# Kernel optimization log

Measured on AMD Instinct MI355X. Metric: run time of the kernel, lower is better.

Reference implementation:

```python
import jax, jax.numpy as jnp
import numpy as np

HIDDEN = 64

def gcn_conv(x, W, b, src, dst, num_nodes):
    # GCNConv: out = D^{-1/2} (A + I) D^{-1/2} (x @ W) + b
    h = x @ W                                            # [N, F_out]
    ones = jnp.ones(src.shape[0], dtype=x.dtype)
    deg = jax.ops.segment_sum(ones, dst, num_segments=num_nodes) + 1.0  # +1 for self-loop
    dinv = jax.lax.rsqrt(deg)                             # deg^{-1/2}, deg >= 1 so safe
    norm = dinv[src] * dinv[dst]                          # [E]
    msgs = h[src] * norm[:, None]                         # [E, F_out]
    agg = jax.ops.segment_sum(msgs, dst, num_segments=num_nodes)
    # self-loop contribution: norm for (i,i) edge = dinv[i]^2
    out = agg + h * (dinv * dinv)[:, None] + b
    return out


def setup_inputs() -> dict:
    key = jax.random.key(0)
    k1, k2, k3, k4, k5 = jax.random.split(key, 5)
    N, F_in, F_out, E = 50000, 256, 128, 1600000
    x = jax.random.normal(k1, (N, F_in), dtype=jnp.float32)
    edge_index = jax.random.randint(k2, (2, E), 0, N, dtype=jnp.int64)
    W1 = jax.random.normal(k3, (F_in, HIDDEN), dtype=jnp.float32) * (1.0 / np.sqrt(F_in))
    b1 = jnp.zeros((HIDDEN,), dtype=jnp.float32)
    W2 = jax.random.normal(k4, (HIDDEN, F_out), dtype=jnp.float32) * (1.0 / np.sqrt(HIDDEN))
    b2 = jnp.zeros((F_out,), dtype=jnp.float32)
    return {"x": x, "edge_index": edge_index, "W1": W1, "b1": b1, "W2": W2, "b2": b2}


def reference(x, edge_index, W1, b1, W2, b2):
    num_nodes = x.shape[0]
    src, dst = edge_index[0], edge_index[1]
    h = gcn_conv(x, W1, b1, src, dst, num_nodes)
    h = jax.nn.relu(h)
    # dropout is identity in eval mode (training=False)
    out = gcn_conv(h, W2, b2, src, dst, num_nodes)
    return out
```

## Files before the change

kernel.cpp:

```cpp
#include <hip/hip_runtime.h>

#define FI 256
#define FH 64
#define FO 128
#define ASORT_CHUNK 2048

__device__ __forceinline__ ushort f2bf(float x) {
    unsigned b = __float_as_uint(x);
    b += 0x7fffu + ((b >> 16) & 1u);
    return (ushort)(b >> 16);
}
__device__ __forceinline__ float bf2f(ushort u) {
    return __uint_as_float(((unsigned)u) << 16);
}


__global__ void zero_i32(int* __restrict__ p, int n) {
    int i = blockIdx.x * 256 + threadIdx.x;
    if (i < n) p[i] = 0;
}

__global__ void deg_cnt_kernel(const int* __restrict__ dst, int* __restrict__ cnt, int E) {
    int base = blockIdx.x * 1024 + threadIdx.x;
    #pragma unroll
    for (int q = 0; q < 4; ++q) {
        int e = base + q * 256;
        if (e < E) atomicAdd(&cnt[dst[e]], 1);
    }
}

__global__ void dinv_kernel(const int* __restrict__ cnt, float* __restrict__ dinv, int N) {
    int i = blockIdx.x * 256 + threadIdx.x;
    if (i < N) dinv[i] = rsqrtf((float)cnt[i] + 1.0f);
}


__global__ __launch_bounds__(256) void hist_part_kernel(const int* __restrict__ dst,
                                                        int* __restrict__ bucket_cnt, int E) {
    __shared__ int lcnt[256];
    int t = threadIdx.x;
    int base = blockIdx.x * ASORT_CHUNK;
    lcnt[t] = 0;
    __syncthreads();
    #pragma unroll
    for (int j = 0; j < 8; ++j) {
        int e = base + j * 256 + t;
        if (e < E) atomicAdd(&lcnt[((unsigned)dst[e]) >> 8], 1);
    }
    __syncthreads();
    int v = lcnt[t];
    if (v > 0) atomicAdd(&bucket_cnt[t], v);
}

__global__ __launch_bounds__(256) void bucket_scan_kernel(const int* __restrict__ bucket_cnt,
                                                          int* __restrict__ bucket_base,
                                                          int* __restrict__ bucket_pos, int E) {
    __shared__ int sc[256];
    int t = threadIdx.x;
    int sum = bucket_cnt[t];
    sc[t] = sum;
    __syncthreads();
    for (int off = 1; off < 256; off <<= 1) {
        int u = (t >= off) ? sc[t - off] : 0;
        __syncthreads();
        sc[t] += u;
        __syncthreads();
    }
    int excl = sc[t] - sum;
    bucket_base[t] = excl;
    bucket_pos[t]  = excl;
    if (t == 255) bucket_base[256] = sc[255];
}

__global__ __launch_bounds__(256) void binA_kernel(const int* __restrict__ src,
                                                   const int* __restrict__ dst,
                                                   int* __restrict__ bucket_pos,
                                                   unsigned* __restrict__ binned, int E) {
    __shared__ int lcnt[256];
    __shared__ int lbase[256];
    __shared__ int gbase[256];
    __shared__ int sc[256];
    __shared__ unsigned sorted[ASORT_CHUNK];
    int t = threadIdx.x;
    int base = blockIdx.x * ASORT_CHUNK;
    lcnt[t] = 0;
    __syncthreads();
    unsigned pk[8];
    short bb[8];
    short mi[8];
    #pragma unroll
    for (int j = 0; j < 8; ++j) {
        int e = base + j * 256 + t;
        if (e < E) {
            unsigned s = (unsigned)src[e];
            unsigned d = (unsigned)dst[e];
            pk[j] = s | (d << 16);
            int b = (int)(d >> 8);
            bb[j] = (short)b;
            mi[j] = (short)atomicAdd(&lcnt[b], 1);
        } else {
            bb[j] = -1;
        }
    }
    __syncthreads();
    int v = lcnt[t];
    sc[t] = v;
    __syncthreads();
    #pragma unroll
    for (int off = 1; off < 256; off <<= 1) {
        int u = (t >= off) ? sc[t - off] : 0;
        __syncthreads();
        sc[t] += u;
        __syncthreads();
    }
    lbase[t] = sc[t] - v;
    if (v > 0) gbase[t] = atomicAdd(&bucket_pos[t], v);
    __syncthreads();
    #pragma unroll
    for (int j = 0; j < 8; ++j)
        if (bb[j] >= 0) sorted[lbase[(int)bb[j]] + (int)mi[j]] = pk[j];
    int tot = sc[255];
    __syncthreads();
    for (int i = t; i < tot; i += 256) {
        unsigned vv = sorted[i];
        int b = (int)(vv >> 24);
        binned[gbase[b] + (i - lbase[b])] = vv;
    }
}

__global__ __launch_bounds__(256) void binB_kernel(const int* __restrict__ bucket_base,
                                                   const unsigned* __restrict__ binned,
                                                   int* __restrict__ rec4,
                                                   int* __restrict__ row_start,
                                                   int* __restrict__ cnt,
                                                   float* __restrict__ dinv, int N) {
    __shared__ int lcnt[256];
    __shared__ int sc[256];
    __shared__ int lstart[256];
    __shared__ int loff[256];
    int t = threadIdx.x;
    int d0 = blockIdx.x << 8;
    int start = bucket_base[blockIdx.x];
    int end   = bucket_base[blockIdx.x + 1];
    lcnt[t] = 0;
    __syncthreads();
    for (int i = start + t; i < end; i += 256)
        atomicAdd(&lcnt[(binned[i] >> 16) & 0xffu], 1);
    __syncthreads();
    int v = lcnt[t];
    sc[t] = v;
    __syncthreads();
    for (int off = 1; off < 256; off <<= 1) {
        int u = (t >= off) ? sc[t - off] : 0;
        __syncthreads();
        sc[t] += u;
        __syncthreads();
    }
    int st = start + sc[t] - v;
    lstart[t] = st;
    loff[t] = 0;
    if (d0 + t < N) {
        row_start[d0 + t] = st;
        cnt[d0 + t] = v;
        dinv[d0 + t] = rsqrtf((float)v + 1.0f);
    }
    __syncthreads();
    int i = start + t;
    for (; i + 768 < end; i += 1024) {
        unsigned v0 = binned[i];
        unsigned v1 = binned[i + 256];
        unsigned v2 = binned[i + 512];
        unsigned v3 = binned[i + 768];
        int dA = (int)((v0 >> 16) & 0xffu); int kA = atomicAdd(&loff[dA], 1);
        rec4[lstart[dA] + kA] = (int)(v0 & 0xffffu);
        int dB = (int)((v1 >> 16) & 0xffu); int kB = atomicAdd(&loff[dB], 1);
        rec4[lstart[dB] + kB] = (int)(v1 & 0xffffu);
        int dC = (int)((v2 >> 16) & 0xffu); int kC = atomicAdd(&loff[dC], 1);
        rec4[lstart[dC] + kC] = (int)(v2 & 0xffffu);
        int dD = (int)((v3 >> 16) & 0xffu); int kD = atomicAdd(&loff[dD], 1);
        rec4[lstart[dD] + kD] = (int)(v3 & 0xffffu);
    }
    for (; i < end; i += 256) {
        unsigned v4 = binned[i];
        int d = (int)((v4 >> 16) & 0xffu);
        int k = atomicAdd(&loff[d], 1);
        rec4[lstart[d] + k] = (int)(v4 & 0xffffu);
    }
}


#define ACC8(hv, wt)                                                   \
    acc[0] = fmaf(__uint_as_float((hv).x << 16),         wt, acc[0]);  \
    acc[1] = fmaf(__uint_as_float((hv).x & 0xffff0000u), wt, acc[1]);  \
    acc[2] = fmaf(__uint_as_float((hv).y << 16),         wt, acc[2]);  \
    acc[3] = fmaf(__uint_as_float((hv).y & 0xffff0000u), wt, acc[3]);  \
    acc[4] = fmaf(__uint_as_float((hv).z << 16),         wt, acc[4]);  \
    acc[5] = fmaf(__uint_as_float((hv).z & 0xffff0000u), wt, acc[5]);  \
    acc[6] = fmaf(__uint_as_float((hv).w << 16),         wt, acc[6]);  \
    acc[7] = fmaf(__uint_as_float((hv).w & 0xffff0000u), wt, acc[7]);

#define GATHER_CHUNK(OFFS)                                                     \
    for (int c0 = 0; c0 < n; c0 += 64) {                                       \
        int idx_l = c0 + L;                                                    \
        int sreg = node;                                                       \
        float wreg = 0.f;                                                      \
        if (idx_l < n) {                                                       \
            sreg = rec4[beg + idx_l];                                          \
            wreg = dinv[sreg] * dvd;                                           \
        }                                                                      \
        int m = n - c0; if (m > 64) m = 64;                                    \
        int umax = (m + 7) >> 3;                                               \
        uint4 hv[8];                                                           \
        _Pragma("unroll")                                                      \
        for (int u = 0; u < 8; ++u) {                                          \
            if (u < umax) {                                                    \
                int sidx = __shfl(sreg, u * 8 + g, 64);                        \
                hv[u] = *(const uint4*)(hb + (size_t)sidx * 256 + (OFFS) + q * 8); \
            }                                                                  \
        }                                                                      \
        _Pragma("unroll")                                                      \
        for (int u = 0; u < 8; ++u) {                                          \
            if (u < umax) {                                                    \
                float wt = __shfl(wreg, u * 8 + g, 64);                        \
                ACC8(hv[u], wt)                                                \
            }                                                                  \
        }                                                                      \
    }

__global__ void gather_relu_kernel(const int* __restrict__ rec4, const int* __restrict__ row_start,
                                   const int* __restrict__ cnt, const float* __restrict__ dinv,
                                   const float* __restrict__ b1, float* __restrict__ out, int N) {
    int node = blockIdx.x * 4 + (threadIdx.x >> 6);
    if (node >= N) return;
    int L = threadIdx.x & 63;
    int g = L >> 3;
    int q = L & 7;
    const ushort* hb = (const ushort*)out;
    int beg = row_start[node];
    int n   = cnt[node];
    float dvd = dinv[node];
    float acc[8] = {0.f, 0.f, 0.f, 0.f, 0.f, 0.f, 0.f, 0.f};
    GATHER_CHUNK(128)
    #pragma unroll
    for (int off = 8; off < 64; off <<= 1)
        #pragma unroll
        for (int j = 0; j < 8; ++j)
            acc[j] += __shfl_xor(acc[j], off, 64);
    if (L < 8) {
        float dv2 = dvd * dvd;
        uint4 ho = *(const uint4*)(hb + (size_t)node * 256 + 128 + q * 8);
        float4 bl = *(const float4*)&b1[q * 8];
        float4 bh = *(const float4*)&b1[q * 8 + 4];
        float r0 = fmaxf(acc[0] + dv2 * __uint_as_float(ho.x << 16)         + bl.x, 0.f);
        float r1 = fmaxf(acc[1] + dv2 * __uint_as_float(ho.x & 0xffff0000u) + bl.y, 0.f);
        float r2 = fmaxf(acc[2] + dv2 * __uint_as_float(ho.y << 16)         + bl.z, 0.f);
        float r3 = fmaxf(acc[3] + dv2 * __uint_as_float(ho.y & 0xffff0000u) + bl.w, 0.f);
        float r4 = fmaxf(acc[4] + dv2 * __uint_as_float(ho.z << 16)         + bh.x, 0.f);
        float r5 = fmaxf(acc[5] + dv2 * __uint_as_float(ho.z & 0xffff0000u) + bh.y, 0.f);
        float r6 = fmaxf(acc[6] + dv2 * __uint_as_float(ho.w << 16)         + bh.z, 0.f);
        float r7 = fmaxf(acc[7] + dv2 * __uint_as_float(ho.w & 0xffff0000u) + bh.w, 0.f);
        uint4 st;
        st.x = (unsigned)f2bf(r0) | ((unsigned)f2bf(r1) << 16);
        st.y = (unsigned)f2bf(r2) | ((unsigned)f2bf(r3) << 16);
        st.z = (unsigned)f2bf(r4) | ((unsigned)f2bf(r5) << 16);
        st.w = (unsigned)f2bf(r6) | ((unsigned)f2bf(r7) << 16);
        *(uint4*)((ushort*)out + (size_t)node * 256 + 192 + q * 8) = st;
    }
}

__global__ void gather_comb_kernel(const int* __restrict__ rec4, const int* __restrict__ row_start,
                                   const int* __restrict__ cnt, const float* __restrict__ dinv,
                                   float* __restrict__ out, int N) {
    int node = blockIdx.x * 4 + (threadIdx.x >> 6);
    if (node >= N) return;
    int L = threadIdx.x & 63;
    int g = L >> 3;
    int q = L & 7;
    const ushort* hb = (const ushort*)out;
    int beg = row_start[node];
    int n   = cnt[node];
    float dvd = dinv[node];
    float acc[8] = {0.f, 0.f, 0.f, 0.f, 0.f, 0.f, 0.f, 0.f};
    GATHER_CHUNK(192)
    #pragma unroll
    for (int off = 8; off < 64; off <<= 1)
        #pragma unroll
        for (int j = 0; j < 8; ++j)
            acc[j] += __shfl_xor(acc[j], off, 64);
    if (L < 8) {
        float dv2 = dvd * dvd;
        uint4 ho = *(const uint4*)(hb + (size_t)node * 256 + 192 + q * 8);
        float4 o0, o1;
        o0.x = acc[0] + dv2 * __uint_as_float(ho.x << 16);
        o0.y = acc[1] + dv2 * __uint_as_float(ho.x & 0xffff0000u);
        o0.z = acc[2] + dv2 * __uint_as_float(ho.y << 16);
        o0.w = acc[3] + dv2 * __uint_as_float(ho.y & 0xffff0000u);
        o1.x = acc[4] + dv2 * __uint_as_float(ho.z << 16);
        o1.y = acc[5] + dv2 * __uint_as_float(ho.z & 0xffff0000u);
        o1.z = acc[6] + dv2 * __uint_as_float(ho.w << 16);
        o1.w = acc[7] + dv2 * __uint_as_float(ho.w & 0xffff0000u);
        *(float4*)&out[(size_t)node * FO + q * 8]     = o0;
        *(float4*)&out[(size_t)node * FO + q * 8 + 4] = o1;
    }
}


__global__ __launch_bounds__(128) void mm1_tiled(const float* __restrict__ x,
                                                 const float* __restrict__ W1,
                                                 float* __restrict__ out, int N) {
    __shared__ float xs[32][128];
    __shared__ float ws[32][64];
    int tid = threadIdx.x;
    int R0  = blockIdx.x * 128;
    int ty  = tid >> 3;
    int tx  = tid & 7;
    float acc[8][8];
    #pragma unroll
    for (int i = 0; i < 8; ++i)
        #pragma unroll
        for (int j = 0; j < 8; ++j) acc[i][j] = 0.f;

    int xrow = R0 + tid;
    bool ok = xrow < N;
    const float* xr = x + (size_t)xrow * FI;
    const float4 z4 = make_float4(0.f, 0.f, 0.f, 0.f);

    float4 xv[8], wv[4];
    #pragma unroll
    for (int i = 0; i < 8; ++i) xv[i] = ok ? *(const float4*)&xr[i * 4] : z4;
    #pragma unroll
    for (int i = 0; i < 4; ++i) {
        int idx = tid * 4 + i;
        wv[i] = *(const float4*)&W1[(size_t)(idx >> 4) * 64 + (idx & 15) * 4];
    }

    for (int t = 0; t < 8; ++t) {
        __syncthreads();
        #pragma unroll
        for (int i = 0; i < 8; ++i) {
            xs[i * 4 + 0][tid] = xv[i].x;
            xs[i * 4 + 1][tid] = xv[i].y;
            xs[i * 4 + 2][tid] = xv[i].z;
            xs[i * 4 + 3][tid] = xv[i].w;
        }
        #pragma unroll
        for (int i = 0; i < 4; ++i) {
            int idx = tid * 4 + i;
            *(float4*)&ws[idx >> 4][(idx & 15) * 4] = wv[i];
        }
        __syncthreads();
        if (t < 7) {
            int k0 = (t + 1) * 32;
            #pragma unroll
            for (int i = 0; i < 8; ++i) xv[i] = ok ? *(const float4*)&xr[k0 + i * 4] : z4;
            #pragma unroll
            for (int i = 0; i < 4; ++i) {
                int idx = tid * 4 + i;
                wv[i] = *(const float4*)&W1[(size_t)(k0 + (idx >> 4)) * 64 + (idx & 15) * 4];
            }
        }
        #pragma unroll 8
        for (int k = 0; k < 32; ++k) {
            float4 al = *(const float4*)&xs[k][ty * 8];
            float4 ah = *(const float4*)&xs[k][ty * 8 + 4];
            float4 bl = *(const float4*)&ws[k][tx * 8];
            float4 bh = *(const float4*)&ws[k][tx * 8 + 4];
            float a[8] = {al.x, al.y, al.z, al.w, ah.x, ah.y, ah.z, ah.w};
            float b[8] = {bl.x, bl.y, bl.z, bl.w, bh.x, bh.y, bh.z, bh.w};
            #pragma unroll
            for (int i = 0; i < 8; ++i)
                #pragma unroll
                for (int j = 0; j < 8; ++j)
                    acc[i][j] = fmaf(a[i], b[j], acc[i][j]);
        }
    }
    #pragma unroll
    for (int i = 0; i < 8; ++i) {
        int row = R0 + ty * 8 + i;
        if (row < N) {
            uint4 st;
            st.x = (unsigned)f2bf(acc[i][0]) | ((unsigned)f2bf(acc[i][1]) << 16);
            st.y = (unsigned)f2bf(acc[i][2]) | ((unsigned)f2bf(acc[i][3]) << 16);
            st.z = (unsigned)f2bf(acc[i][4]) | ((unsigned)f2bf(acc[i][5]) << 16);
            st.w = (unsigned)f2bf(acc[i][6]) | ((unsigned)f2bf(acc[i][7]) << 16);
            *(uint4*)((ushort*)out + (size_t)row * 256 + 128 + tx * 8) = st;
        }
    }
}

__global__ __launch_bounds__(256) void mm2_tiled(const float* __restrict__ W2,
                                                 const float* __restrict__ b2,
                                                 float* __restrict__ out, int N) {
    __shared__ float xs[64][68];
    __shared__ float ws[64][128];
    int tid = threadIdx.x;
    int R0  = blockIdx.x * 64;
    int ty  = tid >> 4;
    int tx  = tid & 15;

    {
        int sr = tid >> 2;
        int l4 = tid & 3;
        int grow = R0 + sr;
        bool ok = grow < N;
        const float* orow = out + (size_t)grow * FO;
        #pragma unroll
        for (int q = 0; q < 4; ++q) {
            int j0 = (l4 + 4 * q) * 4;
            float4 a = ok ? *(const float4*)&orow[j0] : make_float4(0.f, 0.f, 0.f, 0.f);
            xs[j0 + 0][sr] = a.x;
            xs[j0 + 1][sr] = a.y;
            xs[j0 + 2][sr] = a.z;
            xs[j0 + 3][sr] = a.w;
        }
    }
    #pragma unroll
    for (int q = 0; q < 8; ++q) {
        int f = tid + q * 256;
        *(float4*)&ws[f >> 5][(f & 31) * 4] = *(const float4*)&W2[(size_t)f * 4];
    }
    __syncthreads();

    float acc[4][8];
    #pragma unroll
    for (int i = 0; i < 4; ++i)
        #pragma unroll
        for (int j = 0; j < 8; ++j) acc[i][j] = 0.f;

    #pragma unroll 4
    for (int k = 0; k < FH; ++k) {
        float4 a  = *(const float4*)&xs[k][ty * 4];
        float4 bl = *(const float4*)&ws[k][tx * 4];
        float4 bh = *(const float4*)&ws[k][64 + tx * 4];
        float av[4] = {a.x, a.y, a.z, a.w};
        float bv[8] = {bl.x, bl.y, bl.z, bl.w, bh.x, bh.y, bh.z, bh.w};
        #pragma unroll
        for (int i = 0; i < 4; ++i)
            #pragma unroll
            for (int j = 0; j < 8; ++j)
                acc[i][j] = fmaf(av[i], bv[j], acc[i][j]);
    }

    float4 b2l = *(const float4*)&b2[tx * 4];
    float4 b2h = *(const float4*)&b2[64 + tx * 4];
    #pragma unroll
    for (int i = 0; i < 4; ++i) {
        int row = R0 + ty * 4 + i;
        if (row < N) {
            float* o = out + (size_t)row * FO;
            *(float4*)&o[tx * 4] = make_float4(acc[i][0] + b2l.x, acc[i][1] + b2l.y,
                                               acc[i][2] + b2l.z, acc[i][3] + b2l.w);
            *(float4*)&o[64 + tx * 4] = make_float4(acc[i][4] + b2h.x, acc[i][5] + b2h.y,
                                                    acc[i][6] + b2h.z, acc[i][7] + b2h.w);
        }
    }
}


__global__ void expand_hs1_kernel(float* __restrict__ out, int N) {
    int row = blockIdx.x * 4 + (threadIdx.x >> 6);
    if (row >= N) return;
    int lane = threadIdx.x & 63;
    float v = bf2f(((const ushort*)out)[(size_t)row * 256 + 128 + lane]);
    out[(size_t)row * FO + FH + lane] = v;
}

__global__ void zero_half_kernel(float* __restrict__ out, int half, int N) {
    int i = blockIdx.x * 256 + threadIdx.x;
    if (i >= N * FH) return;
    out[(size_t)(i >> 6) * FO + half + (i & 63)] = 0.f;
}

__global__ void scatter_half_kernel(const int* __restrict__ src, const int* __restrict__ dst,
                                    const float* __restrict__ dinv, float* __restrict__ out,
                                    int rh, int wh, int E) {
    int e = blockIdx.x * 4 + (threadIdx.x >> 6);
    if (e >= E) return;
    int lane = threadIdx.x & 63;
    int s = src[e];
    int d = dst[e];
    float w = dinv[s] * dinv[d];
    atomicAdd(&out[(size_t)d * FO + wh + lane], out[(size_t)s * FO + rh + lane] * w);
}

__global__ void finish1_kernel(float* __restrict__ out, const float* __restrict__ dinv,
                               const float* __restrict__ b1, int N) {
    int i = blockIdx.x * 256 + threadIdx.x;
    if (i >= N * FH) return;
    int row = i >> 6;
    int c   = i & 63;
    size_t base = (size_t)row * FO;
    float dv = dinv[row];
    out[base + c] = fmaxf(out[base + c] + dv * dv * out[base + FH + c] + b1[c], 0.f);
}

__global__ void finish2_kernel(float* __restrict__ out, const float* __restrict__ dinv, int N) {
    int i = blockIdx.x * 256 + threadIdx.x;
    if (i >= N * FH) return;
    int row = i >> 6;
    int c   = i & 63;
    size_t base = (size_t)row * FO;
    float dv = dinv[row];
    out[base + c] = out[base + FH + c] + dv * dv * out[base + c];
}

extern "C" void kernel_launch(void* const* d_in, const int* in_sizes, int n_in,
                              void* d_out, int out_size, void* d_ws, size_t ws_size,
                              hipStream_t stream) {
    const float* x  = (const float*)d_in[0];
    const int*   ei = (const int*)d_in[1];
    const float* W1 = (const float*)d_in[2];
    const float* b1 = (const float*)d_in[3];
    const float* W2 = (const float*)d_in[4];
    const float* b2 = (const float*)d_in[5];
    float* out = (float*)d_out;

    int N = in_sizes[0] / FI;
    int E = in_sizes[1] / 2;
    const int* src = ei;
    const int* dst = ei + E;

    char* w = (char*)d_ws;
    float* dinv        = (float*)w;      w += (size_t)N * 4;
    int*   cnt         = (int*)w;        w += (size_t)N * 4;
    int*   row_start   = (int*)w;        w += (size_t)N * 4;
    int*   bucket_cnt  = (int*)w;        w += 256 * 4;
    int*   bucket_pos  = (int*)w;        w += 256 * 4;
    int*   bucket_base = (int*)w;        w += 260 * 4;
    unsigned* binned   = (unsigned*)w;   w += (size_t)E * 4;
    int*   rec4        = (int*)w;        w += (size_t)E * 4;
    size_t need = (size_t)(w - (char*)d_ws);

    int nblkA = (E + ASORT_CHUNK - 1) / ASORT_CHUNK;
    int nbk   = (N + 255) >> 8;

    if (ws_size >= need && N <= 65536) {
        zero_i32<<<1, 256, 0, stream>>>(bucket_cnt, 256);
        hist_part_kernel<<<nblkA, 256, 0, stream>>>(dst, bucket_cnt, E);
        bucket_scan_kernel<<<1, 256, 0, stream>>>(bucket_cnt, bucket_base, bucket_pos, E);
        binA_kernel<<<nblkA, 256, 0, stream>>>(src, dst, bucket_pos, binned, E);
        binB_kernel<<<nbk, 256, 0, stream>>>(bucket_base, binned, rec4, row_start, cnt, dinv, N);

        mm1_tiled<<<(N + 127) / 128, 128, 0, stream>>>(x, W1, out, N);
        gather_relu_kernel<<<(N + 3) / 4, 256, 0, stream>>>(rec4, row_start, cnt, dinv, b1, out, N);
        gather_comb_kernel<<<(N + 3) / 4, 256, 0, stream>>>(rec4, row_start, cnt, dinv, out, N);
        mm2_tiled<<<(N + 63) / 64, 256, 0, stream>>>(W2, b2, out, N);
    } else {
        zero_i32<<<(N + 255) / 256, 256, 0, stream>>>(cnt, N);
        deg_cnt_kernel<<<(E + 1023) / 1024, 256, 0, stream>>>(dst, cnt, E);
        dinv_kernel<<<(N + 255) / 256, 256, 0, stream>>>(cnt, dinv, N);
        mm1_tiled<<<(N + 127) / 128, 128, 0, stream>>>(x, W1, out, N);
        expand_hs1_kernel<<<(N + 3) / 4, 256, 0, stream>>>(out, N);
        zero_half_kernel<<<((N * FH) + 255) / 256, 256, 0, stream>>>(out, 0, N);
        scatter_half_kernel<<<(E + 3) / 4, 256, 0, stream>>>(src, dst, dinv, out, FH, 0, E);
        finish1_kernel<<<((N * FH) + 255) / 256, 256, 0, stream>>>(out, dinv, b1, N);
        zero_half_kernel<<<((N * FH) + 255) / 256, 256, 0, stream>>>(out, FH, N);
        scatter_half_kernel<<<(E + 3) / 4, 256, 0, stream>>>(src, dst, dinv, out, 0, FH, E);
        finish2_kernel<<<((N * FH) + 255) / 256, 256, 0, stream>>>(out, dinv, N);
        mm2_tiled<<<(N + 63) / 64, 256, 0, stream>>>(W2, b2, out, N);
    }
}
```

Before: 311.4 us.

## Replace FP32 FMA tiled first matmul with split-bf16 MFMA kernel

Rewrites the x@W1 kernel to use bf16 MFMA instructions, splitting each fp32 operand into high and low bf16 parts and running three MFMAs per tile to keep near-fp32 accuracy. W1 is converted and pre-laid out in shared memory once per block, and x is read straight from global into registers without shared staging. The aim is to move the matmul from scalar FMA onto matrix cores. In exchange every block redundantly converts all of W1, and the output stores become scattered 2-byte writes.

```diff
diff --git a/kernel.cpp b/kernel.cpp
--- a/kernel.cpp
+++ b/kernel.cpp
@@ -4,6 +4,9 @@
 #define FH 64
 #define FO 128
 #define ASORT_CHUNK 2048
+
+typedef __attribute__((ext_vector_type(8))) short bf16x8;
+typedef __attribute__((ext_vector_type(4))) float f32x4;
 
 __device__ __forceinline__ ushort f2bf(float x) {
     unsigned b = __float_as_uint(x);
@@ -305,85 +308,91 @@
 }
 
 
-__global__ __launch_bounds__(128) void mm1_tiled(const float* __restrict__ x,
-                                                 const float* __restrict__ W1,
-                                                 float* __restrict__ out, int N) {
-    __shared__ float xs[32][128];
-    __shared__ float ws[32][64];
+__global__ __launch_bounds__(256) void mm1_mfma(const float* __restrict__ x,
+                                                const float* __restrict__ W1,
+                                                float* __restrict__ out, int N) {
+    __shared__ short bfH[2048 * 8];
+    __shared__ short bfL[2048 * 8];
     int tid = threadIdx.x;
+
+    for (int e = tid; e < 2048; e += 256) {
+        int l  = e & 63;
+        int ct = e >> 6;
+        int c  = ct >> 3, t = ct & 7;
+        int col = c * 16 + (l & 15);
+        int kb  = t * 32 + (l >> 4) * 8;
+        #pragma unroll
+        for (int j = 0; j < 8; ++j) {
+            float wv = W1[(size_t)(kb + j) * 64 + col];
+            ushort h = f2bf(wv);
+            bfH[e * 8 + j] = (short)h;
+            bfL[e * 8 + j] = (short)f2bf(wv - bf2f(h));
+        }
+    }
+    __syncthreads();
+
+    int wid = tid >> 6;
+    int l   = tid & 63;
     int R0  = blockIdx.x * 128;
-    int ty  = tid >> 3;
-    int tx  = tid & 7;
-    float acc[8][8];
-    #pragma unroll
-    for (int i = 0; i < 8; ++i)
-        #pragma unroll
-        for (int j = 0; j < 8; ++j) acc[i][j] = 0.f;
-
-    int xrow = R0 + tid;
-    bool ok = xrow < N;
-    const float* xr = x + (size_t)xrow * FI;
+    int rowA = R0 + wid * 32 + (l & 15);
+    int rowB = rowA + 16;
+    int kg   = l >> 4;
+    const float* xrA = x + (size_t)rowA * FI;
+    const float* xrB = x + (size_t)rowB * FI;
+    bool okA = rowA < N, okB = rowB < N;
     const float4 z4 = make_float4(0.f, 0.f, 0.f, 0.f);
 
-    float4 xv[8], wv[4];
-    #pragma unroll
-    for (int i = 0; i < 8; ++i) xv[i] = ok ? *(const float4*)&xr[i * 4] : z4;
-    #pragma unroll
-    for (int i = 0; i < 4; ++i) {
-        int idx = tid * 4 + i;
-        wv[i] = *(const float4*)&W1[(size_t)(idx >> 4) * 64 + (idx & 15) * 4];
-    }
+    f32x4 acc[2][4];
+    #pragma unroll
+    for (int i = 0; i < 2; ++i)
+        #pragma unroll
+        for (int c = 0; c < 4; ++c) acc[i][c] = (f32x4){0.f, 0.f, 0.f, 0.f};
 
     for (int t = 0; t < 8; ++t) {
-        __syncthreads();
-        #pragma unroll
-        for (int i = 0; i < 8; ++i) {
-            xs[i * 4 + 0][tid] = xv[i].x;
-            xs[i * 4 + 1][tid] = xv[i].y;
-            xs[i * 4 + 2][tid] = xv[i].z;
-            xs[i * 4 + 3][tid] = xv[i].w;
-        }
-        #pragma unroll
-        for (int i = 0; i < 4; ++i) {
-            int idx = tid * 4 + i;
-            *(float4*)&ws[idx >> 4][(idx & 15) * 4] = wv[i];
-        }
-        __syncthreads();
-        if (t < 7) {
-            int k0 = (t + 1) * 32;
+        int kb = t * 32 + kg * 8;
+        float4 a0 = okA ? *(const float4*)&xrA[kb]     : z4;
+        float4 a1 = okA ? *(const float4*)&xrA[kb + 4] : z4;
+        float4 b0 = okB ? *(const float4*)&xrB[kb]     : z4;
+        float4 b1 = okB ? *(const float4*)&xrB[kb + 4] : z4;
+        bf16x8 ahA, alA, ahB, alB;
+        {
+            float va[8] = {a0.x, a0.y, a0.z, a0.w, a1.x, a1.y, a1.z, a1.w};
+            float vb[8] = {b0.x, b0.y, b0.z, b0.w, b1.x, b1.y, b1.z, b1.w};
             #pragma unroll
-            for (int i = 0; i < 8; ++i) xv[i] = ok ? *(const float4*)&xr[k0 + i * 4] : z4;
-            #pragma unroll
-            for (int i = 0; i < 4; ++i) {
-                int idx = tid * 4 + i;
-                wv[i] = *(const float4*)&W1[(size_t)(k0 + (idx >> 4)) * 64 + (idx & 15) * 4];
+            for (int j = 0; j < 8; ++j) {
+                ushort h1v = f2bf(va[j]);
+                ahA[j] = (short)h1v;
+                alA[j] = (short)f2bf(va[j] - bf2f(h1v));
+                ushort h2v = f2bf(vb[j]);
+                ahB[j] = (short)h2v;
+                alB[j] = (short)f2bf(vb[j] - bf2f(h2v));
             }
         }
-        #pragma unroll 8
-        for (int k = 0; k < 32; ++k) {
-            float4 al = *(const float4*)&xs[k][ty * 8];
-            float4 ah = *(const float4*)&xs[k][ty * 8 + 4];
-            float4 bl = *(const float4*)&ws[k][tx * 8];
-            float4 bh = *(const float4*)&ws[k][tx * 8 + 4];
-            float a[8] = {al.x, al.y, al.z, al.w, ah.x, ah.y, ah.z, ah.w};
-            float b[8] = {bl.x, bl.y, bl.z, bl.w, bh.x, bh.y, bh.z, bh.w};
-            #pragma unroll
-            for (int i = 0; i < 8; ++i)
+        #pragma unroll
+        for (int c = 0; c < 4; ++c) {
+            int e = (c * 8 + t) * 64 + l;
+            bf16x8 bh = *(const bf16x8*)&bfH[e * 8];
+            bf16x8 bl = *(const bf16x8*)&bfL[e * 8];
+            acc[0][c] = __builtin_amdgcn_mfma_f32_16x16x32_bf16(ahA, bh, acc[0][c], 0, 0, 0);
+            acc[0][c] = __builtin_amdgcn_mfma_f32_16x16x32_bf16(ahA, bl, acc[0][c], 0, 0, 0);
+            acc[0][c] = __builtin_amdgcn_mfma_f32_16x16x32_bf16(alA, bh, acc[0][c], 0, 0, 0);
+            acc[1][c] = __builtin_amdgcn_mfma_f32_16x16x32_bf16(ahB, bh, acc[1][c], 0, 0, 0);
+            acc[1][c] = __builtin_amdgcn_mfma_f32_16x16x32_bf16(ahB, bl, acc[1][c], 0, 0, 0);
+            acc[1][c] = __builtin_amdgcn_mfma_f32_16x16x32_bf16(alB, bh, acc[1][c], 0, 0, 0);
+        }
+    }
+    #pragma unroll
+    for (int i = 0; i < 2; ++i) {
+        int rbase = R0 + wid * 32 + i * 16 + (l >> 4) * 4;
+        #pragma unroll
+        for (int r = 0; r < 4; ++r) {
+            int row = rbase + r;
+            if (row < N) {
+                ushort* ob = (ushort*)out + (size_t)row * 256 + 128;
                 #pragma unroll
-                for (int j = 0; j < 8; ++j)
-                    acc[i][j] = fmaf(a[i], b[j], acc[i][j]);
-        }
-    }
-    #pragma unroll
-    for (int i = 0; i < 8; ++i) {
-        int row = R0 + ty * 8 + i;
-        if (row < N) {
-            uint4 st;
-            st.x = (unsigned)f2bf(acc[i][0]) | ((unsigned)f2bf(acc[i][1]) << 16);
-            st.y = (unsigned)f2bf(acc[i][2]) | ((unsigned)f2bf(acc[i][3]) << 16);
-            st.z = (unsigned)f2bf(acc[i][4]) | ((unsigned)f2bf(acc[i][5]) << 16);
-            st.w = (unsigned)f2bf(acc[i][6]) | ((unsigned)f2bf(acc[i][7]) << 16);
-            *(uint4*)((ushort*)out + (size_t)row * 256 + 128 + tx * 8) = st;
+                for (int c = 0; c < 4; ++c)
+                    ob[c * 16 + (l & 15)] = f2bf(acc[i][c][r]);
+            }
         }
     }
 }
@@ -541,7 +550,7 @@
         binA_kernel<<<nblkA, 256, 0, stream>>>(src, dst, bucket_pos, binned, E);
         binB_kernel<<<nbk, 256, 0, stream>>>(bucket_base, binned, rec4, row_start, cnt, dinv, N);
 
-        mm1_tiled<<<(N + 127) / 128, 128, 0, stream>>>(x, W1, out, N);
+        mm1_mfma<<<(N + 127) / 128, 256, 0, stream>>>(x, W1, out, N);
         gather_relu_kernel<<<(N + 3) / 4, 256, 0, stream>>>(rec4, row_start, cnt, dinv, b1, out, N);
         gather_comb_kernel<<<(N + 3) / 4, 256, 0, stream>>>(rec4, row_start, cnt, dinv, out, N);
         mm2_tiled<<<(N + 63) / 64, 256, 0, stream>>>(W2, b2, out, N);
@@ -549,7 +558,7 @@
         zero_i32<<<(N + 255) / 256, 256, 0, stream>>>(cnt, N);
         deg_cnt_kernel<<<(E + 1023) / 1024, 256, 0, stream>>>(dst, cnt, E);
         dinv_kernel<<<(N + 255) / 256, 256, 0, stream>>>(cnt, dinv, N);
-        mm1_tiled<<<(N + 127) / 128, 128, 0, stream>>>(x, W1, out, N);
+        mm1_mfma<<<(N + 127) / 128, 256, 0, stream>>>(x, W1, out, N);
         expand_hs1_kernel<<<(N + 3) / 4, 256, 0, stream>>>(out, N);
         zero_half_kernel<<<((N * FH) + 255) / 256, 256, 0, stream>>>(out, 0, N);
         scatter_half_kernel<<<(E + 3) / 4, 256, 0, stream>>>(src, dst, dinv, out, FH, 0, E);
```

Measured after the change: 277.5 us. -10.9%, faster.
